# Performance work log

Measured on AMD Instinct MI355X. Metric: run time of the kernel, lower is better.

Reference implementation:

```python
import jax, jax.numpy as jnp
import numpy as np

B, N, E = 32, 196, 1024          # batch, encoder tokens, encoder feature dim
D = 1024                          # decoder_token_size
V = 32000                         # vocab_size
T = 100                           # max_tokens_during_train
START = 0                         # start_token_id


def setup_inputs() -> dict:
    key = jax.random.key(0)
    ks = jax.random.split(key, 16)
    s = 0.02
    return {
        "features": jax.random.normal(ks[0], (B, N, E), jnp.float32),
        # features_attn_head: ReLU -> Linear(E, D)
        "W_fk": jax.random.normal(ks[1], (E, D), jnp.float32) * s,
        "b_fk": jnp.zeros((D,), jnp.float32),
        # features_values: ReLU -> Linear(E, D)
        "W_fv": jax.random.normal(ks[2], (E, D), jnp.float32) * s,
        "b_fv": jnp.zeros((D,), jnp.float32),
        # text_features_attn_head: ReLU -> Linear(D, D)
        "W_tk": jax.random.normal(ks[3], (D, D), jnp.float32) * s,
        "b_tk": jnp.zeros((D,), jnp.float32),
        # LSTMCell(D, D): gates ordered [i, f, g, o]
        "W_ih": jax.random.normal(ks[4], (D, 4 * D), jnp.float32) * s,
        "W_hh": jax.random.normal(ks[5], (D, 4 * D), jnp.float32) * s,
        "b_ih": jnp.zeros((4 * D,), jnp.float32),
        "b_hh": jnp.zeros((4 * D,), jnp.float32),
        # lm_head: Linear(D, V)
        "W_lm": jax.random.normal(ks[6], (D, V), jnp.float32) * s,
        "b_lm": jnp.zeros((V,), jnp.float32),
        # bos token embedding (text_embedding(start_token_id)), detached in fwd
        "bos_embed": jax.random.normal(ks[7], (D,), jnp.float32) * s,
    }


def reference(features, W_fk, b_fk, W_fv, b_fv, W_tk, b_tk,
              W_ih, W_hh, b_ih, b_hh, W_lm, b_lm, bos_embed):
    scale = jnp.sqrt(jnp.asarray(D, jnp.float32))
    # encoder-side projections (constant over decode steps)
    context_key = jax.nn.relu(features) @ W_fk + b_fk      # [B, N, D]
    context_values = jax.nn.relu(features) @ W_fv + b_fv   # [B, N, D]

    h0 = jnp.broadcast_to(jax.lax.stop_gradient(bos_embed)[None, :], (B, D))
    c0 = jnp.zeros((B, D), jnp.float32)

    def step(carry, _):
        h, c = carry
        # input_values = hidden_state.detach().clone()
        q_in = jax.lax.stop_gradient(h)
        seq_keys = jax.nn.relu(q_in) @ W_tk + b_tk          # [B, D]
        # scaled_dot_product_attention(context_key, seq_keys[:,None,:], context_values)
        dot = jnp.einsum('bnd,bd->bn', context_key, seq_keys)[..., None] / scale  # [B,N,1]
        attn = jax.nn.softmax(dot, axis=-1)                 # softmax over size-1 dim -> ones
        ctx = jnp.einsum('bn,bnd->bd', attn[..., 0], context_values)  # [B, D]
        # torch LSTMCell
        gates = ctx @ W_ih + h @ W_hh + b_ih + b_hh         # [B, 4D]
        i_, f_, g_, o_ = jnp.split(gates, 4, axis=-1)
        c_new = jax.nn.sigmoid(f_) * c + jax.nn.sigmoid(i_) * jnp.tanh(g_)
        h_new = jax.nn.sigmoid(o_) * jnp.tanh(c_new)
        logits = h_new @ W_lm + b_lm                        # [B, V]
        return (h_new, c_new), logits

    _, logits_seq = jax.lax.scan(step, (h0, c0), None, length=T - 1)  # [T-1, B, V]
    first = jnp.zeros((1, B, V), jnp.float32).at[0, :, START].set(1.0)
    return jnp.concatenate([first, logits_seq], axis=0)    # [T, B, V]
```

## Files before the change

### kernel.cpp

```cpp
#include <hip/hip_runtime.h>
#include <hip/hip_bf16.h>
#include <stdint.h>

typedef __attribute__((ext_vector_type(8))) short short8;
typedef __attribute__((ext_vector_type(4))) float f32x4;

#define B_ 32
#define N_ 196
#define D_ 1024
#define V_ 32000
#define NSTEP 99
#define MROWS 3168
#define MPAD  3200
#define SENT  0x7FC07FC07FC07FC0ULL

#define OFF_WT     0ULL
#define OFF_H      65536000ULL
#define OFF_FSUM   72089600ULL
#define OFF_CTXP   72220672ULL
#define OFF_GBASEP 72482816ULL

#define AS3 __attribute__((address_space(3)))
#define AS1 __attribute__((address_space(1)))
static __device__ __forceinline__ void gload_lds16(const void* g, void* l) {
  __builtin_amdgcn_global_load_lds((const AS1 uint32_t*)g, (AS3 uint32_t*)l, 16, 0, 0);
}

__global__ void k_fsum(const float* __restrict__ feat, float* __restrict__ fsum,
                       unsigned long long* __restrict__ Hq) {
  if (blockIdx.x >= 128) {
    int gid = (blockIdx.x - 128) * 256 + threadIdx.x;
    for (int w = gid; w < NSTEP * 8192; w += 65536) Hq[w] = SENT;
    return;
  }
  int idx = blockIdx.x * 256 + threadIdx.x;
  int b = idx >> 10, e = idx & 1023;
  const float* p = feat + (size_t)b * (N_ * D_) + e;
  float s = 0.f;
  #pragma unroll 4
  for (int n = 0; n < N_; ++n) s += fmaxf(p[(size_t)n * D_], 0.f);
  fsum[idx] = s;
}

__global__ void k_ctx(const float* __restrict__ fsum, const float* __restrict__ W_fv,
                      const float* __restrict__ b_fv, float* __restrict__ ctxp) {
  __shared__ float fs[16][512];
  int kc = blockIdx.z;
  int e0 = kc * 512;
  int b0 = blockIdx.y * 16;
  int d = blockIdx.x * 64 + (threadIdx.x & 63);
  int bq = threadIdx.x >> 6;
  for (int i = threadIdx.x; i < 8192; i += 256)
    fs[i >> 9][i & 511] = fsum[(b0 + (i >> 9)) * 1024 + e0 + (i & 511)];
  __syncthreads();
  float bias = (kc == 0) ? 196.f * b_fv[d] : 0.f;
  float acc[4] = {bias, bias, bias, bias};
  for (int e4 = 0; e4 < 128; ++e4) {
    float w0 = W_fv[(size_t)(e0 + 4 * e4 + 0) * 1024 + d];
    float w1 = W_fv[(size_t)(e0 + 4 * e4 + 1) * 1024 + d];
    float w2 = W_fv[(size_t)(e0 + 4 * e4 + 2) * 1024 + d];
    float w3 = W_fv[(size_t)(e0 + 4 * e4 + 3) * 1024 + d];
    #pragma unroll
    for (int r = 0; r < 4; ++r) {
      float4 c = *(const float4*)&fs[bq * 4 + r][e4 * 4];
      acc[r] = fmaf(c.x, w0, fmaf(c.y, w1, fmaf(c.z, w2, fmaf(c.w, w3, acc[r]))));
    }
  }
  #pragma unroll
  for (int r = 0; r < 4; ++r)
    ctxp[kc * 32768 + (size_t)(b0 + bq * 4 + r) * 1024 + d] = acc[r];
}

__global__ void k_gbase(const float* __restrict__ ctxp, const float* __restrict__ W_ih,
                        const float* __restrict__ b_ih, const float* __restrict__ b_hh,
                        float* __restrict__ gbasep) {
  __shared__ float cs[16][256];
  int kc = blockIdx.z;
  int e0 = kc * 256;
  int b0 = blockIdx.y * 16;
  int j = blockIdx.x * 256 + threadIdx.x;
  for (int i = threadIdx.x; i < 4096; i += 256) {
    int r = i >> 8, e = i & 255;
    cs[r][e] = ctxp[(size_t)(b0 + r) * 1024 + e0 + e]
             + ctxp[32768 + (size_t)(b0 + r) * 1024 + e0 + e];
  }
  __syncthreads();
  float bias = (kc == 0) ? (b_ih[j] + b_hh[j]) : 0.f;
  float acc[16];
  #pragma unroll
  for (int r = 0; r < 16; ++r) acc[r] = bias;
  for (int e4 = 0; e4 < 64; ++e4) {
    float w0 = W_ih[(size_t)(e0 + 4 * e4 + 0) * 4096 + j];
    float w1 = W_ih[(size_t)(e0 + 4 * e4 + 1) * 4096 + j];
    float w2 = W_ih[(size_t)(e0 + 4 * e4 + 2) * 4096 + j];
    float w3 = W_ih[(size_t)(e0 + 4 * e4 + 3) * 4096 + j];
    #pragma unroll
    for (int r = 0; r < 16; ++r) {
      float4 c = *(const float4*)&cs[r][e4 * 4];
      acc[r] = fmaf(c.x, w0, fmaf(c.y, w1, fmaf(c.z, w2, fmaf(c.w, w3, acc[r]))));
    }
  }
  #pragma unroll
  for (int r = 0; r < 16; ++r)
    gbasep[kc * 131072 + (size_t)(b0 + r) * 4096 + j] = acc[r];
}

__global__ __launch_bounds__(256, 1) void k_rec(
    const float* __restrict__ gbasep, const float* __restrict__ W_hh,
    const float* __restrict__ bos, unsigned long long* __restrict__ Hq,
    const float* __restrict__ W_lm, __hip_bfloat16* __restrict__ WT,
    float* __restrict__ out) {
  extern __shared__ char lds[];
  const int tid = threadIdx.x;
  const int blk = blockIdx.x;

  if (blk >= 128) {
    __hip_bfloat16* t = (__hip_bfloat16*)lds;
    int wblk = blk - 128;
    for (int idx = wblk * 256 + tid; idx < B_ * V_; idx += 128 * 256)
      __builtin_nontemporal_store(((idx % V_) == 0) ? 1.0f : 0.0f, &out[idx]);
    if (wblk < 64) ((uint32_t*)(Hq + (size_t)MROWS * 256))[wblk * 256 + tid] = 0u;
    int tx = tid & 63, ty = tid >> 6;
    int word = tx & 31, nh = tx >> 5;
    for (int tile = wblk; tile < 8000; tile += 128) {
      int k0 = (tile & 15) * 64;
      int n0 = (tile >> 4) * 64;
      __syncthreads();
      #pragma unroll
      for (int i = 0; i < 16; ++i) {
        int r = i * 4 + ty;
        t[r * 66 + tx] = __float2bfloat16(
            __builtin_nontemporal_load(&W_lm[(size_t)(k0 + r) * V_ + n0 + tx]));
      }
      __syncthreads();
      #pragma unroll
      for (int i = 0; i < 8; ++i) {
        int n = i * 8 + ty * 2 + nh;
        uint32_t lo = *(const uint16_t*)&t[2 * word * 66 + n];
        uint32_t hi = *(const uint16_t*)&t[(2 * word + 1) * 66 + n];
        __builtin_nontemporal_store(lo | (hi << 16),
            (uint32_t*)&WT[(size_t)(n0 + n) * 1024 + k0] + word);
      }
    }
    return;
  }

  __hip_bfloat16* hbuf = (__hip_bfloat16*)lds;
  __hip_bfloat16* wbuf = (__hip_bfloat16*)(lds + 32768);
  float* gexb = (float*)(lds + 32768);

  const int bh = blk >> 6;
  const int dg = blk & 63;

  for (int idx = tid; idx < 64 * 1024; idx += 256) {
    int c = idx & 63;
    int k = idx >> 6;
    float w = W_hh[(size_t)k * 4096 + (c >> 4) * 1024 + dg * 16 + (c & 15)];
    wbuf[c * 1024 + ((((k >> 3) ^ (c & 7)) << 3) | (k & 7))] = __float2bfloat16(w);
  }
  for (int idx = tid; idx < 16 * 1024; idx += 256) {
    int row = idx >> 10;
    int k = idx & 1023;
    hbuf[row * 1024 + ((((k >> 3) ^ (row & 7)) << 3) | (k & 7))] = __float2bfloat16(bos[k]);
  }

  const int btl = tid >> 4;
  const int dl = tid & 15;
  float gb0 = 0.f, gb1 = 0.f, gb2 = 0.f, gb3 = 0.f;
  #pragma unroll
  for (int kc = 0; kc < 4; ++kc) {
    size_t base = (size_t)kc * 131072 + (size_t)(bh * 16 + btl) * 4096 + dg * 16 + dl;
    gb0 += gbasep[base + 0 * 1024];
    gb1 += gbasep[base + 1 * 1024];
    gb2 += gbasep[base + 2 * 1024];
    gb3 += gbasep[base + 3 * 1024];
  }
  float cst = 0.f;

  const int lane = tid & 63;
  const int wid = tid >> 6;
  const int arow = lane & 15;
  const int bcol = wid * 16 + (lane & 15);
  const int kg = lane >> 4;
  const int axor = arow & 7;

  __syncthreads();

  short8 breg[32];
  #pragma unroll
  for (int kt = 0; kt < 32; ++kt) {
    int ca = kt * 4 + kg;
    breg[kt] = *(const short8*)&wbuf[bcol * 1024 + ((ca ^ (bcol & 7)) << 3)];
  }

  const int pubw = (bh * 16 + btl) * 256 + dg * 4 + (dl >> 2);

  for (int t = 0; t < NSTEP; ++t) {
    float* gex = gexb + (t & 1) * (16 * 68);
    f32x4 acc0 = {0.f, 0.f, 0.f, 0.f};
    f32x4 acc1 = {0.f, 0.f, 0.f, 0.f};
    #pragma unroll
    for (int kt = 0; kt < 32; kt += 2) {
      int ca = kt * 4 + kg;
      short8 a0 = *(const short8*)&hbuf[arow * 1024 + ((ca ^ axor) << 3)];
      acc0 = __builtin_amdgcn_mfma_f32_16x16x32_bf16(a0, breg[kt], acc0, 0, 0, 0);
      short8 a1 = *(const short8*)&hbuf[arow * 1024 + (((ca + 4) ^ axor) << 3)];
      acc1 = __builtin_amdgcn_mfma_f32_16x16x32_bf16(a1, breg[kt + 1], acc1, 0, 0, 0);
    }
    acc0 = acc0 + acc1;
    {
      int bq = (lane >> 4) << 2;
      #pragma unroll
      for (int q = 0; q < 4; ++q) gex[(bq + q) * 68 + bcol] = acc0[q];
    }
    __syncthreads();

    float gi = gex[btl * 68 + 0  + dl] + gb0;
    float gf = gex[btl * 68 + 16 + dl] + gb1;
    float gg = gex[btl * 68 + 32 + dl] + gb2;
    float go = gex[btl * 68 + 48 + dl] + gb3;
    float si = 1.f / (1.f + __expf(-gi));
    float sf = 1.f / (1.f + __expf(-gf));
    float so = 1.f / (1.f + __expf(-go));
    cst = sf * cst + si * tanhf(gg);
    float h = so * tanhf(cst);

    float h1 = __shfl_down(h, 1);
    float h2 = __shfl_down(h, 2);
    float h3 = __shfl_down(h, 3);
    if ((dl & 3) == 0) {
      __hip_bfloat16 q0 = __float2bfloat16(h), q1 = __float2bfloat16(h1);
      __hip_bfloat16 q2 = __float2bfloat16(h2), q3 = __float2bfloat16(h3);
      unsigned long long v = (unsigned long long)*(uint16_t*)&q0
                           | ((unsigned long long)*(uint16_t*)&q1 << 16)
                           | ((unsigned long long)*(uint16_t*)&q2 << 32)
                           | ((unsigned long long)*(uint16_t*)&q3 << 48);
      __hip_atomic_store(&Hq[(size_t)t * 8192 + pubw], v,
                         __ATOMIC_RELAXED, __HIP_MEMORY_SCOPE_AGENT);
    }

    if (t == NSTEP - 1) break;

    {
      const unsigned long long* src = Hq + (size_t)t * 8192 + (size_t)bh * 16 * 256;
      for (;;) {
        unsigned long long v[16];
        #pragma unroll
        for (int j = 0; j < 16; ++j)
          v[j] = __hip_atomic_load(&src[j * 256 + tid],
                                   __ATOMIC_RELAXED, __HIP_MEMORY_SCOPE_AGENT);
        int nready = 0;
        #pragma unroll
        for (int j = 0; j < 16; ++j) {
          if (v[j] != SENT) {
            int off = (((tid >> 1) ^ (j & 7)) << 3) + ((tid & 1) << 2);
            *(uint2*)&hbuf[j * 1024 + off] = *(uint2*)&v[j];
            ++nready;
          }
        }
        if (nready == 16) break;
        __builtin_amdgcn_s_sleep(1);
      }
    }
    __syncthreads();
  }
}

__global__ __launch_bounds__(1024, 1) void k_gemm(
    const __hip_bfloat16* __restrict__ H,
    const __hip_bfloat16* __restrict__ WT,
    const float* __restrict__ b_lm,
    float* __restrict__ out) {
  extern __shared__ char glds[];
  __hip_bfloat16* As = (__hip_bfloat16*)glds;
  __hip_bfloat16* Bs = (__hip_bfloat16*)(glds + 65536);

  int bid = blockIdx.x;
  int xcd = bid & 7;
  int idx = bid >> 3;
  int wg = (xcd < 1 ? xcd * 204 : 204 + (xcd - 1) * 203) + idx;
  int nt = wg / 13;
  int mt = wg - nt * 13;
  const int mbase = mt * 256;
  const int nbase = nt * 256;

  const int tid = threadIdx.x;
  const int lane = tid & 63;
  const int wid = tid >> 6;
  const int wm = wid >> 2;
  const int wn = wid & 3;

  f32x4 acc[4][4];
  #pragma unroll
  for (int m = 0; m < 4; ++m)
    #pragma unroll
    for (int n = 0; n < 4; ++n) acc[m][n] = (f32x4){0.f, 0.f, 0.f, 0.f};

  const int kg = lane >> 4;

  int srowA[2], srowB[2], soff[2];
  #pragma unroll
  for (int j = 0; j < 2; ++j) {
    int c = j * 1024 + tid;
    int row = c >> 3;
    srowB[j] = nbase + row;
    srowA[j] = min(mbase + row, MPAD - 1);
    soff[j] = ((c & 7) ^ (row & 7)) * 8;
  }
  const int ldsbase = (tid & 960) * 8;

  auto STAGE = [&](int nb, int kt) {
    #pragma unroll
    for (int j = 0; j < 2; ++j)
      gload_lds16(H + (size_t)srowA[j] * 1024 + kt * 64 + soff[j],
                  As + nb * 16384 + j * 8192 + ldsbase);
    #pragma unroll
    for (int j = 0; j < 2; ++j)
      gload_lds16(WT + (size_t)srowB[j] * 1024 + kt * 64 + soff[j],
                  Bs + nb * 16384 + j * 8192 + ldsbase);
  };
  auto COMPUTE = [&](int nb) {
    __builtin_amdgcn_s_setprio(1);
    #pragma unroll
    for (int kk = 0; kk < 2; ++kk) {
      const int slot = kk * 4 + kg;
      short8 a[4], b[4];
      #pragma unroll
      for (int m = 0; m < 4; ++m) {
        int r = wm * 64 + m * 16 + (lane & 15);
        a[m] = *(const short8*)&As[nb * 16384 + r * 64 + ((slot ^ (r & 7)) << 3)];
      }
      #pragma unroll
      for (int n = 0; n < 4; ++n) {
        int r = wn * 64 + n * 16 + (lane & 15);
        b[n] = *(const short8*)&Bs[nb * 16384 + r * 64 + ((slot ^ (r & 7)) << 3)];
      }
      #pragma unroll
      for (int m = 0; m < 4; ++m)
        #pragma unroll
        for (int n = 0; n < 4; ++n)
          acc[m][n] = __builtin_amdgcn_mfma_f32_16x16x32_bf16(a[m], b[n], acc[m][n], 0, 0, 0);
    }
    __builtin_amdgcn_s_setprio(0);
  };

  STAGE(0, 0);
  asm volatile("s_waitcnt vmcnt(0)" ::: "memory");
  __builtin_amdgcn_s_barrier();
  for (int kt = 0; kt < 16; ++kt) {
    if (kt < 15) STAGE((kt + 1) & 1, kt + 1);
    COMPUTE(kt & 1);
    asm volatile("s_waitcnt vmcnt(0)" ::: "memory");
    __builtin_amdgcn_s_barrier();
  }

  if (mt != 12) {
    #pragma unroll
    for (int n = 0; n < 4; ++n) {
      int gcol = nbase + wn * 64 + n * 16 + (lane & 15);
      float bl = b_lm[gcol];
      #pragma unroll
      for (int m = 0; m < 4; ++m) {
        int rbase = mbase + wm * 64 + m * 16 + ((lane >> 4) << 2);
        #pragma unroll
        for (int q = 0; q < 4; ++q)
          __builtin_nontemporal_store(acc[m][n][q] + bl,
              &out[(size_t)(rbase + q + 32) * V_ + gcol]);
      }
    }
  } else {
    #pragma unroll
    for (int n = 0; n < 4; ++n) {
      int gcol = nbase + wn * 64 + n * 16 + (lane & 15);
      float bl = b_lm[gcol];
      #pragma unroll
      for (int m = 0; m < 4; ++m) {
        int rbase = mbase + wm * 64 + m * 16 + ((lane >> 4) << 2);
        #pragma unroll
        for (int q = 0; q < 4; ++q) {
          int r = rbase + q;
          if (r < MROWS)
            __builtin_nontemporal_store(acc[m][n][q] + bl,
                &out[(size_t)(r + 32) * V_ + gcol]);
        }
      }
    }
  }
}

extern "C" void kernel_launch(void* const* d_in, const int* in_sizes, int n_in,
                              void* d_out, int out_size, void* d_ws, size_t ws_size,
                              hipStream_t stream) {
  const float* features = (const float*)d_in[0];
  const float* W_fv = (const float*)d_in[3];
  const float* b_fv = (const float*)d_in[4];
  const float* W_ih = (const float*)d_in[7];
  const float* W_hh = (const float*)d_in[8];
  const float* b_ih = (const float*)d_in[9];
  const float* b_hh = (const float*)d_in[10];
  const float* W_lm = (const float*)d_in[11];
  const float* b_lm = (const float*)d_in[12];
  const float* bos  = (const float*)d_in[13];
  float* out = (float*)d_out;
  char* ws = (char*)d_ws;

  __hip_bfloat16* WT     = (__hip_bfloat16*)(ws + OFF_WT);
  __hip_bfloat16* H      = (__hip_bfloat16*)(ws + OFF_H);
  unsigned long long* Hq = (unsigned long long*)(ws + OFF_H);
  float* fsum            = (float*)(ws + OFF_FSUM);
  float* ctxp            = (float*)(ws + OFF_CTXP);
  float* gbasep          = (float*)(ws + OFF_GBASEP);

  hipLaunchKernelGGL(k_fsum,  dim3(384),       dim3(256), 0, stream, features, fsum, Hq);
  hipLaunchKernelGGL(k_ctx,   dim3(16, 2, 2),  dim3(256), 0, stream, fsum, W_fv, b_fv, ctxp);
  hipLaunchKernelGGL(k_gbase, dim3(16, 2, 4),  dim3(256), 0, stream, ctxp, W_ih, b_ih, b_hh, gbasep);
  hipLaunchKernelGGL(k_rec,   dim3(256),  dim3(256), 163840, stream,
                     gbasep, W_hh, bos, Hq, W_lm, WT, out);
  hipLaunchKernelGGL(k_gemm,  dim3(1625), dim3(1024), 131072, stream, H, WT, b_lm, out);
}
```

Baseline: 749.1 us.

## Repartition LSTM recurrence blocks to 8 batch rows by 32 hidden units

The recurrent kernel now uses 512 threads per block. Each of the 128 recurrence blocks owns 8 batch rows (the MFMA tile's other 8 rows are zero-padded) and 32 hidden units, where before it owned 16 rows and 16 units. Each block therefore polls and copies only 8 rows of the published hidden state per step, spreads the W_hh slice across 8 waves, and runs the gate math on half the threads. The aim is to shorten the per-step cross-block synchronisation and h-gather latency. The cost is wasted MFMA work on the padding rows, more LDS staging rounds, and the W_lm transpose side blocks running at a different width.

```diff
diff --git a/kernel.cpp b/kernel.cpp
--- a/kernel.cpp
+++ b/kernel.cpp
@@ -105,7 +105,7 @@
     gbasep[kc * 131072 + (size_t)(b0 + r) * 4096 + j] = acc[r];
 }
 
-__global__ __launch_bounds__(256, 1) void k_rec(
+__global__ __launch_bounds__(512, 1) void k_rec(
     const float* __restrict__ gbasep, const float* __restrict__ W_hh,
     const float* __restrict__ bos, unsigned long long* __restrict__ Hq,
     const float* __restrict__ W_lm, __hip_bfloat16* __restrict__ WT,
@@ -113,13 +113,15 @@
   extern __shared__ char lds[];
   const int tid = threadIdx.x;
   const int blk = blockIdx.x;
+  const int lane = tid & 63;
+  const int wid = tid >> 6;
 
   if (blk >= 128) {
     __hip_bfloat16* t = (__hip_bfloat16*)lds;
     int wblk = blk - 128;
-    for (int idx = wblk * 256 + tid; idx < B_ * V_; idx += 128 * 256)
+    for (int idx = wblk * 512 + tid; idx < B_ * V_; idx += 128 * 512)
       __builtin_nontemporal_store(((idx % V_) == 0) ? 1.0f : 0.0f, &out[idx]);
-    if (wblk < 64) ((uint32_t*)(Hq + (size_t)MROWS * 256))[wblk * 256 + tid] = 0u;
+    if (wblk < 16) Hq[(size_t)MROWS * 256 + wblk * 512 + tid] = 0ULL;
     int tx = tid & 63, ty = tid >> 6;
     int word = tx & 31, nh = tx >> 5;
     for (int tile = wblk; tile < 8000; tile += 128) {
@@ -127,15 +129,15 @@
       int n0 = (tile >> 4) * 64;
       __syncthreads();
       #pragma unroll
-      for (int i = 0; i < 16; ++i) {
-        int r = i * 4 + ty;
+      for (int i = 0; i < 8; ++i) {
+        int r = i * 8 + ty;
         t[r * 66 + tx] = __float2bfloat16(
             __builtin_nontemporal_load(&W_lm[(size_t)(k0 + r) * V_ + n0 + tx]));
       }
       __syncthreads();
       #pragma unroll
-      for (int i = 0; i < 8; ++i) {
-        int n = i * 8 + ty * 2 + nh;
+      for (int i = 0; i < 4; ++i) {
+        int n = i * 16 + ty * 2 + nh;
         uint32_t lo = *(const uint16_t*)&t[2 * word * 66 + n];
         uint32_t hi = *(const uint16_t*)&t[(2 * word + 1) * 66 + n];
         __builtin_nontemporal_store(lo | (hi << 16),
@@ -149,54 +151,61 @@
   __hip_bfloat16* wbuf = (__hip_bfloat16*)(lds + 32768);
   float* gexb = (float*)(lds + 32768);
 
-  const int bh = blk >> 6;
-  const int dg = blk & 63;
-
-  for (int idx = tid; idx < 64 * 1024; idx += 256) {
-    int c = idx & 63;
-    int k = idx >> 6;
-    float w = W_hh[(size_t)k * 4096 + (c >> 4) * 1024 + dg * 16 + (c & 15)];
-    wbuf[c * 1024 + ((((k >> 3) ^ (c & 7)) << 3) | (k & 7))] = __float2bfloat16(w);
-  }
-  for (int idx = tid; idx < 16 * 1024; idx += 256) {
+  const int bq = blk >> 5;
+  const int dg = blk & 31;
+
+  for (int idx = tid; idx < 16 * 1024; idx += 512) {
     int row = idx >> 10;
     int k = idx & 1023;
-    hbuf[row * 1024 + ((((k >> 3) ^ (row & 7)) << 3) | (k & 7))] = __float2bfloat16(bos[k]);
-  }
-
-  const int btl = tid >> 4;
-  const int dl = tid & 15;
-  float gb0 = 0.f, gb1 = 0.f, gb2 = 0.f, gb3 = 0.f;
-  #pragma unroll
-  for (int kc = 0; kc < 4; ++kc) {
-    size_t base = (size_t)kc * 131072 + (size_t)(bh * 16 + btl) * 4096 + dg * 16 + dl;
-    gb0 += gbasep[base + 0 * 1024];
-    gb1 += gbasep[base + 1 * 1024];
-    gb2 += gbasep[base + 2 * 1024];
-    gb3 += gbasep[base + 3 * 1024];
-  }
-  float cst = 0.f;
-
-  const int lane = tid & 63;
-  const int wid = tid >> 6;
+    float v = (row < 8) ? bos[k] : 0.f;
+    hbuf[row * 1024 + ((((k >> 3) ^ (row & 7)) << 3) | (k & 7))] = __float2bfloat16(v);
+  }
+
   const int arow = lane & 15;
   const int bcol = wid * 16 + (lane & 15);
   const int kg = lane >> 4;
   const int axor = arow & 7;
 
+  short8 breg[32];
+#define WROUND(R)                                                                   \
+  __syncthreads();                                                                  \
+  for (int idx = tid; idx < 65536; idx += 512) {                                    \
+    int c = idx & 127;                                                              \
+    int kk = idx >> 7;                                                              \
+    float w = W_hh[(size_t)((R) * 512 + kk) * 4096 + (c >> 5) * 1024 + dg * 32 + (c & 31)]; \
+    wbuf[c * 512 + ((((kk >> 3) ^ (c & 7)) << 3) | (kk & 7))] = __float2bfloat16(w); \
+  }                                                                                 \
+  __syncthreads();                                                                  \
+  _Pragma("unroll")                                                                 \
+  for (int j = 0; j < 16; ++j) {                                                    \
+    int ck = j * 4 + kg;                                                            \
+    breg[(R) * 16 + j] = *(const short8*)&wbuf[bcol * 512 + ((ck ^ (bcol & 7)) << 3)]; \
+  }
+  WROUND(0)
+  WROUND(1)
+#undef WROUND
+
+  const int btl = tid >> 5;
+  const int dl = tid & 31;
+  float gb0 = 0.f, gb1 = 0.f, gb2 = 0.f, gb3 = 0.f;
+  if (tid < 256) {
+    #pragma unroll
+    for (int kc = 0; kc < 4; ++kc) {
+      size_t base = (size_t)kc * 131072 + (size_t)(bq * 8 + btl) * 4096 + dg * 32 + dl;
+      gb0 += gbasep[base + 0 * 1024];
+      gb1 += gbasep[base + 1 * 1024];
+      gb2 += gbasep[base + 2 * 1024];
+      gb3 += gbasep[base + 3 * 1024];
+    }
+  }
+  float cst = 0.f;
+
+  const int pubw = (bq * 8 + (btl & 7)) * 256 + dg * 8 + (dl >> 2);
+
   __syncthreads();
 
-  short8 breg[32];
-  #pragma unroll
-  for (int kt = 0; kt < 32; ++kt) {
-    int ca = kt * 4 + kg;
-    breg[kt] = *(const short8*)&wbuf[bcol * 1024 + ((ca ^ (bcol & 7)) << 3)];
-  }
-
-  const int pubw = (bh * 16 + btl) * 256 + dg * 4 + (dl >> 2);
-
   for (int t = 0; t < NSTEP; ++t) {
-    float* gex = gexb + (t & 1) * (16 * 68);
+    float* gex = gexb + (t & 1) * (16 * 132);
     f32x4 acc0 = {0.f, 0.f, 0.f, 0.f};
     f32x4 acc1 = {0.f, 0.f, 0.f, 0.f};
     #pragma unroll
@@ -209,56 +218,60 @@
     }
     acc0 = acc0 + acc1;
     {
-      int bq = (lane >> 4) << 2;
-      #pragma unroll
-      for (int q = 0; q < 4; ++q) gex[(bq + q) * 68 + bcol] = acc0[q];
+      int brow = (lane >> 4) << 2;
+      #pragma unroll
+      for (int q = 0; q < 4; ++q) gex[(brow + q) * 132 + bcol] = acc0[q];
     }
     __syncthreads();
 
-    float gi = gex[btl * 68 + 0  + dl] + gb0;
-    float gf = gex[btl * 68 + 16 + dl] + gb1;
-    float gg = gex[btl * 68 + 32 + dl] + gb2;
-    float go = gex[btl * 68 + 48 + dl] + gb3;
-    float si = 1.f / (1.f + __expf(-gi));
-    float sf = 1.f / (1.f + __expf(-gf));
-    float so = 1.f / (1.f + __expf(-go));
-    cst = sf * cst + si * tanhf(gg);
-    float h = so * tanhf(cst);
-
-    float h1 = __shfl_down(h, 1);
-    float h2 = __shfl_down(h, 2);
-    float h3 = __shfl_down(h, 3);
-    if ((dl & 3) == 0) {
-      __hip_bfloat16 q0 = __float2bfloat16(h), q1 = __float2bfloat16(h1);
-      __hip_bfloat16 q2 = __float2bfloat16(h2), q3 = __float2bfloat16(h3);
-      unsigned long long v = (unsigned long long)*(uint16_t*)&q0
-                           | ((unsigned long long)*(uint16_t*)&q1 << 16)
-                           | ((unsigned long long)*(uint16_t*)&q2 << 32)
-                           | ((unsigned long long)*(uint16_t*)&q3 << 48);
-      __hip_atomic_store(&Hq[(size_t)t * 8192 + pubw], v,
-                         __ATOMIC_RELAXED, __HIP_MEMORY_SCOPE_AGENT);
+    if (tid < 256) {
+      float gi = gex[btl * 132 + 0  + dl] + gb0;
+      float gf = gex[btl * 132 + 32 + dl] + gb1;
+      float gg = gex[btl * 132 + 64 + dl] + gb2;
+      float go = gex[btl * 132 + 96 + dl] + gb3;
+      float si = 1.f / (1.f + __expf(-gi));
+      float sf = 1.f / (1.f + __expf(-gf));
+      float so = 1.f / (1.f + __expf(-go));
+      cst = sf * cst + si * tanhf(gg);
+      float h = so * tanhf(cst);
+
+      float h1 = __shfl_down(h, 1);
+      float h2 = __shfl_down(h, 2);
+      float h3 = __shfl_down(h, 3);
+      if ((dl & 3) == 0) {
+        __hip_bfloat16 q0 = __float2bfloat16(h), q1 = __float2bfloat16(h1);
+        __hip_bfloat16 q2 = __float2bfloat16(h2), q3 = __float2bfloat16(h3);
+        unsigned long long v = (unsigned long long)*(uint16_t*)&q0
+                             | ((unsigned long long)*(uint16_t*)&q1 << 16)
+                             | ((unsigned long long)*(uint16_t*)&q2 << 32)
+                             | ((unsigned long long)*(uint16_t*)&q3 << 48);
+        __hip_atomic_store(&Hq[(size_t)t * 8192 + pubw], v,
+                           __ATOMIC_RELAXED, __HIP_MEMORY_SCOPE_AGENT);
+      }
     }
 
     if (t == NSTEP - 1) break;
 
     {
-      const unsigned long long* src = Hq + (size_t)t * 8192 + (size_t)bh * 16 * 256;
+      const unsigned long long* src = Hq + (size_t)t * 8192 + (size_t)bq * 8 * 256;
       for (;;) {
-        unsigned long long v[16];
+        unsigned long long v[4];
         #pragma unroll
-        for (int j = 0; j < 16; ++j)
-          v[j] = __hip_atomic_load(&src[j * 256 + tid],
+        for (int j = 0; j < 4; ++j)
+          v[j] = __hip_atomic_load(&src[j * 512 + tid],
                                    __ATOMIC_RELAXED, __HIP_MEMORY_SCOPE_AGENT);
         int nready = 0;
         #pragma unroll
-        for (int j = 0; j < 16; ++j) {
+        for (int j = 0; j < 4; ++j) {
           if (v[j] != SENT) {
-            int off = (((tid >> 1) ^ (j & 7)) << 3) + ((tid & 1) << 2);
-            *(uint2*)&hbuf[j * 1024 + off] = *(uint2*)&v[j];
+            int w = j * 512 + tid;
+            int row = w >> 8, c = w & 255;
+            int off = (((c >> 1) ^ (row & 7)) << 3) + ((c & 1) << 2);
+            *(uint2*)&hbuf[row * 1024 + off] = *(uint2*)&v[j];
             ++nready;
           }
         }
-        if (nready == 16) break;
+        if (nready == 4) break;
         __builtin_amdgcn_s_sleep(1);
       }
     }
@@ -414,7 +427,7 @@
   hipLaunchKernelGGL(k_fsum,  dim3(384),       dim3(256), 0, stream, features, fsum, Hq);
   hipLaunchKernelGGL(k_ctx,   dim3(16, 2, 2),  dim3(256), 0, stream, fsum, W_fv, b_fv, ctxp);
   hipLaunchKernelGGL(k_gbase, dim3(16, 2, 4),  dim3(256), 0, stream, ctxp, W_ih, b_ih, b_hh, gbasep);
-  hipLaunchKernelGGL(k_rec,   dim3(256),  dim3(256), 163840, stream,
+  hipLaunchKernelGGL(k_rec,   dim3(256),  dim3(512), 163840, stream,
                      gbasep, W_hh, bos, Hq, W_lm, WT, out);
   hipLaunchKernelGGL(k_gemm,  dim3(1625), dim3(1024), 131072, stream, H, WT, b_lm, out);
 }
```

New measurement: 686.4 us. 8.4% less time.
